# Kernel tuning notes

Hardware: AMD Instinct MI355X
Metric: run time of the kernel (lower is better)

The kernel has to match this reference:

```python
import jax, jax.numpy as jnp
import numpy as np

B, DIM, Hs, Ws_ = 16, 96, 112, 112
HEADS, WS, OUT = 3, 7, 96
DH = OUT // HEADS


def _rel_index(ws):
    ch = np.arange(ws)
    coords = np.stack(np.meshgrid(ch, ch, indexing='ij'), 0).reshape(2, -1)
    rel = (coords[:, :, None] - coords[:, None, :]).transpose(1, 2, 0).copy()
    rel[..., 0] += ws - 1
    rel[..., 1] += ws - 1
    rel[..., 0] *= 2 * ws - 1
    return rel.sum(-1)  # [ws*ws, ws*ws]


def grid_sample_zeros(img, grid):
    # img [N,C,H,W], grid [N,Hg,Wg,2] with (x,y) in [-1,1]; bilinear, align_corners=True, zeros padding
    N, C, H, W = img.shape
    x = (grid[..., 0] + 1.0) * 0.5 * (W - 1)
    y = (grid[..., 1] + 1.0) * 0.5 * (H - 1)
    x0 = jnp.floor(x); y0 = jnp.floor(y)
    x1 = x0 + 1.0; y1 = y0 + 1.0
    wa = (x1 - x) * (y1 - y); wb = (x - x0) * (y1 - y)
    wc = (x1 - x) * (y - y0); wd = (x - x0) * (y - y0)

    def gather(ix, iy):
        valid = ((ix >= 0) & (ix <= W - 1) & (iy >= 0) & (iy <= H - 1)).astype(img.dtype)
        ixc = jnp.clip(ix, 0, W - 1).astype(jnp.int32)
        iyc = jnp.clip(iy, 0, H - 1).astype(jnp.int32)
        vals = jax.vmap(lambda im, yy, xx: im[:, yy, xx])(img, iyc, ixc)  # [N,C,Hg,Wg]
        return vals * valid[:, None, :, :]

    return (gather(x0, y0) * wa[:, None] + gather(x1, y0) * wb[:, None]
            + gather(x0, y1) * wc[:, None] + gather(x1, y1) * wd[:, None])


def setup_inputs() -> dict:
    key = jax.random.key(0)
    ks = jax.random.split(key, 8)
    s = 0.02
    return {
        'x': jax.random.normal(ks[0], (B, DIM, Hs, Ws_), jnp.float32),
        'w_qkv': jax.random.normal(ks[1], (3 * OUT, DIM), jnp.float32) * s,
        'b_qkv': jnp.zeros((3 * OUT,), jnp.float32),
        'w_off': jax.random.normal(ks[2], (2 * HEADS, DIM), jnp.float32) * s,
        'b_off': jnp.zeros((2 * HEADS,), jnp.float32),
        'w_scl': jax.random.normal(ks[3], (2 * HEADS, DIM), jnp.float32) * s,
        'b_scl': jnp.zeros((2 * HEADS,), jnp.float32),
        'rpb': jax.random.normal(ks[4], ((2 * WS - 1) ** 2, HEADS), jnp.float32) * s,
        'w_proj': jax.random.normal(ks[5], (OUT, OUT), jnp.float32) * s,
        'b_proj': jnp.zeros((OUT,), jnp.float32),
    }


def _forward(x, w_qkv, b_qkv, w_off, b_off, w_scl, b_scl, rpb, w_proj, b_proj):
    b, C, h, w = x.shape
    ws, H, dh = WS, HEADS, DH
    scale = (C // H) ** -0.5
    pad_td = (ws - h % ws) % ws; pad_lr = (ws - w % ws) % ws
    pt, pd = pad_td // 2, pad_td - pad_td // 2
    pl, pr = pad_lr // 2, pad_lr - pad_lr // 2
    eh, ew = h + pad_td, w + pad_lr
    wnh, wnw = eh // ws, ew // ws
    xp = jnp.pad(x, ((0, 0), (0, 0), (pt, pd), (pl, pr)))

    # base reference grid, channel 0 = x (width), channel 1 = y (height)
    irh = jnp.linspace(-1.0, 1.0, eh); irw = jnp.linspace(-1.0, 1.0, ew)
    base = jnp.stack([jnp.broadcast_to(irw[None, :], (eh, ew)),
                      jnp.broadcast_to(irh[:, None], (eh, ew))], 0).reshape(2, wnh, ws, wnw, ws)
    bch = jnp.arange(ws) * 2.0 / (eh - 1); bch = bch - bch.mean()
    bcw = jnp.arange(ws) * 2.0 / (ew - 1); bcw = bcw - bcw.mean()
    wc = jnp.stack([jnp.broadcast_to(bcw[None, None, None, :], (wnh, ws, wnw, ws)),
                    jnp.broadcast_to(bch[None, :, None, None], (wnh, ws, wnw, ws))], 0)

    # per-window offset / scale prediction: avgpool(ws) -> leaky_relu -> 1x1 conv
    pooled = xp.reshape(b, C, wnh, ws, wnw, ws).mean(axis=(3, 5))
    act = jax.nn.leaky_relu(pooled)  # slope 0.01, matches torch default
    off = (jnp.einsum('bchw,oc->bohw', act, w_off) + b_off[None, :, None, None]).reshape(b * H, 2, wnh, wnw)
    off = jnp.stack([off[:, 0] / (h // ws), off[:, 1] / (w // ws)], 1)
    scl = (jnp.einsum('bchw,oc->bohw', act, w_scl) + b_scl[None, :, None, None]).reshape(b * H, 2, wnh, wnw)

    coords = base[None] + wc[None] * scl[:, :, :, None, :, None] + off[:, :, :, None, :, None]
    grid = coords.transpose(0, 2, 3, 4, 5, 1).reshape(b * H, eh, ew, 2)

    qkv = jnp.einsum('bchw,oc->bohw', x, w_qkv) + b_qkv[None, :, None, None]
    qkv = qkv.reshape(b, 3, H, dh, h, w).transpose(1, 0, 2, 3, 4, 5).reshape(3 * b * H, dh, h, w)
    qkv = jnp.pad(qkv, ((0, 0), (0, 0), (pt, pd), (pl, pr))).reshape(3, b * H, dh, eh, ew)
    q, k, v = qkv[0], qkv[1], qkv[2]

    k_s = grid_sample_zeros(k, grid)
    v_s = grid_sample_zeros(v, grid)

    def to_win(t):  # [b*H, dh, eh, ew] -> [b*wnh*wnw, H, ws*ws, dh]
        return t.reshape(b, H, dh, wnh, ws, wnw, ws).transpose(0, 3, 5, 1, 4, 6, 2).reshape(b * wnh * wnw, H, ws * ws, dh)

    qw, kw, vw = to_win(q), to_win(k_s), to_win(v_s)
    dots = jnp.einsum('wnqd,wnkd->wnqk', qw, kw) * scale
    rel_idx = jnp.asarray(_rel_index(ws))
    bias = rpb[rel_idx.reshape(-1)].reshape(ws * ws, ws * ws, H).transpose(2, 0, 1)
    attn = jax.nn.softmax(dots + bias[None], axis=-1)
    out = jnp.einsum('wnqk,wnkd->wnqd', attn, vw)
    out = out.reshape(b, wnh, wnw, H, ws, ws, dh).transpose(0, 3, 6, 1, 4, 2, 5).reshape(b, H * dh, eh, ew)
    out = out[:, :, pt:h + pt, pl:w + pl]
    out = jnp.einsum('bchw,oc->bohw', out, w_proj) + b_proj[None, :, None, None]
    return out


def reference(x, w_qkv, b_qkv, w_off, b_off, w_scl, b_scl, rpb, w_proj, b_proj):
    return _forward(x, w_qkv, b_qkv, w_off, b_off, w_scl, b_scl, rpb, w_proj, b_proj)
```

## Files before the change

kernel.cpp:

```cpp
#include <hip/hip_runtime.h>
#include <hip/hip_bf16.h>
#include <stdint.h>

#define NB 16
#define CDIM 96
#define HW 112
#define NPOS (HW*HW)
#define NHEAD 3
#define DH 32
#define WN 16
#define NWIN (WN*WN)
#define SCALE 0.17677669529663687f

typedef __attribute__((ext_vector_type(8))) short bf16x8;
typedef __attribute__((ext_vector_type(4))) float f32x4;

__device__ __forceinline__ float bfbits_lo(uint32_t w){ union{uint32_t u; float f;} a; a.u = w<<16; return a.f; }
__device__ __forceinline__ float bfbits_hi(uint32_t w){ union{uint32_t u; float f;} a; a.u = w & 0xFFFF0000u; return a.f; }
__device__ __forceinline__ uint32_t packbf(float x, float y){
  union{float f; uint32_t u;} a, b; a.f = x; b.f = y;
  uint32_t ua = a.u + 0x7FFFu + ((a.u>>16)&1u);
  uint32_t ub = b.u + 0x7FFFu + ((b.u>>16)&1u);
  return (ua>>16) | (ub & 0xFFFF0000u);
}
__device__ __forceinline__ unsigned short f2bf(float x){
  union{float f; uint32_t u;} a; a.f = x;
  return (unsigned short)((a.u + 0x7FFFu + ((a.u>>16)&1u))>>16);
}

__global__ void k_pool_act(const float* __restrict__ x, float* __restrict__ act){
  int n = blockIdx.x*256 + threadIdx.x;
  int ww = n & 15; int wh = (n>>4)&15; int bc = n>>8;
  const float* src = x + (size_t)bc*NPOS + (size_t)(wh*7)*HW + ww*7;
  float s = 0.f;
  #pragma unroll
  for (int r=0;r<7;r++){
    const float* row = src + r*HW;
    s += row[0]+row[1]+row[2]+row[3]+row[4]+row[5]+row[6];
  }
  s *= (1.f/49.f);
  act[n] = s > 0.f ? s : 0.01f*s;
}

__global__ void k_offscl(const float* __restrict__ act,
                         const float* __restrict__ woff, const float* __restrict__ boff,
                         const float* __restrict__ wscl, const float* __restrict__ bscl,
                         float4* __restrict__ offscl){
  int n = blockIdx.x*256 + threadIdx.x;
  int b = n >> 8; int wpos = n & 255;
  float accO[6], accS[6];
  #pragma unroll
  for (int o=0;o<6;o++){ accO[o]=boff[o]; accS[o]=bscl[o]; }
  const float* a = act + (size_t)b*CDIM*NWIN + wpos;
  for (int c=0;c<CDIM;c++){
    float av = a[(size_t)c*NWIN];
    #pragma unroll
    for (int o=0;o<6;o++){ accO[o] += av*woff[o*CDIM+c]; accS[o] += av*wscl[o*CDIM+c]; }
  }
  #pragma unroll
  for (int h=0;h<NHEAD;h++){
    float4 r;
    r.x = accO[2*h]   * (1.f/16.f);
    r.y = accO[2*h+1] * (1.f/16.f);
    r.z = accS[2*h];
    r.w = accS[2*h+1];
    offscl[(size_t)(b*NHEAD+h)*NWIN + wpos] = r;
  }
}

__global__ void k_bias_pre(const float* __restrict__ rpb, float* __restrict__ bias_g){
  int n = blockIdx.x*256 + threadIdx.x;
  if (n >= 3*64*64) return;
  int h = n >> 12; int q = (n>>6)&63; int k = n&63;
  float v = -1e30f;
  if (k < 49){
    int qc = q < 49 ? q : 48;
    int qi = qc/7, qj = qc - (qc/7)*7;
    int ki = k/7,  kj = k - (k/7)*7;
    v = rpb[((qi-ki+6)*13 + (qj-kj+6))*3 + h];
  }
  bias_g[n] = v;
}

__launch_bounds__(256)
__global__ void k_qkv_mfma(const float* __restrict__ x, const float* __restrict__ wqkv,
                           const float* __restrict__ bqkv,
                           unsigned short* __restrict__ q, unsigned short* __restrict__ kk,
                           unsigned short* __restrict__ v){
  __shared__ float xf[96*72];
  __shared__ uint4 xbf4[64*13];
  __shared__ uint4 wbf4[96*13];
  const int t = threadIdx.x;
  const int b = blockIdx.x / 196;
  const int p0 = (blockIdx.x % 196) * 64;

  #pragma unroll
  for (int i=0;i<6;i++){
    int f = t + i*256; int c = f>>4; int p4 = (f&15)*4;
    *(float4*)(xf + c*72 + p4) = *(const float4*)(x + (size_t)(b*CDIM+c)*NPOS + p0 + p4);
  }
  __syncthreads();
  #pragma unroll
  for (int i=0;i<3;i++){
    int u = t + i*256; int pos = u & 63; int oct = u >> 6;
    uint32_t pk0 = packbf(xf[(oct*8+0)*72+pos], xf[(oct*8+1)*72+pos]);
    uint32_t pk1 = packbf(xf[(oct*8+2)*72+pos], xf[(oct*8+3)*72+pos]);
    uint32_t pk2 = packbf(xf[(oct*8+4)*72+pos], xf[(oct*8+5)*72+pos]);
    uint32_t pk3 = packbf(xf[(oct*8+6)*72+pos], xf[(oct*8+7)*72+pos]);
    xbf4[pos*13 + oct] = make_uint4(pk0,pk1,pk2,pk3);
  }

  const int lane = t & 63, wv = t >> 6;
  const int g = lane >> 4, r16 = lane & 15;

  for (int s=0;s<3;s++){
    if (s) __syncthreads();
    #pragma unroll
    for (int i=0;i<9;i++){
      int f = t + i*256; int o = f/24; int c4m = f%24;
      float4 wvv = *(const float4*)(wqkv + (size_t)(s*96+o)*CDIM + c4m*4);
      ((uint2*)wbf4)[o*26 + c4m] = make_uint2(packbf(wvv.x,wvv.y), packbf(wvv.z,wvv.w));
    }
    __syncthreads();

    f32x4 acc[6];
    #pragma unroll
    for (int nf=0;nf<6;nf++) acc[nf] = (f32x4){0.f,0.f,0.f,0.f};
    #pragma unroll
    for (int ks=0;ks<3;ks++){
      bf16x8 a = *(const bf16x8*)&xbf4[(wv*16 + r16)*13 + ks*4 + g];
      #pragma unroll
      for (int nf=0;nf<6;nf++){
        bf16x8 bb = *(const bf16x8*)&wbf4[(nf*16 + r16)*13 + ks*4 + g];
        acc[nf] = __builtin_amdgcn_mfma_f32_16x16x32_bf16(a, bb, acc[nf], 0,0,0);
      }
    }
    unsigned short* dst = (s==0)?q:((s==1)?kk:v);
    float sc = (s==0) ? SCALE : 1.f;
    #pragma unroll
    for (int nf=0;nf<6;nf++){
      int o = nf*16 + r16; int h = o>>5; int d = o&31;
      float bv = bqkv[s*96+o];
      size_t base = ((size_t)(b*NHEAD+h)*NPOS + p0 + wv*16 + g*4)*DH + d;
      #pragma unroll
      for (int rr=0;rr<4;rr++)
        dst[base + (size_t)rr*DH] = f2bf((acc[nf][rr] + bv)*sc);
    }
  }
}

__launch_bounds__(128)
__global__ void k_attn_mfma(const unsigned short* __restrict__ qb,
                            const unsigned short* __restrict__ kb,
                            const unsigned short* __restrict__ vb,
                            const float4* __restrict__ offscl,
                            const float* __restrict__ bias_g,
                            float* __restrict__ aout){
  __shared__ unsigned short lds_u[2*8192];
  const int h   = blockIdx.x % 3;
  const int grp = blockIdx.x / 3;
  const int wv  = threadIdx.x >> 6;
  const int lane = threadIdx.x & 63;
  const int win = grp*2 + wv;
  const int b = win>>8, wh=(win>>4)&15, ww=win&15;
  const int bh = b*NHEAD + h;
  const int g = lane>>4, r16 = lane&15;

  unsigned short* K_s  = lds_u + wv*8192;
  unsigned short* VT_s = lds_u + wv*8192 + 2048;
  unsigned short* P_s  = lds_u + wv*8192 + 4096;

  uint4 qf[4];
  #pragma unroll
  for (int qt=0;qt<4;qt++){
    int qq = qt*16 + r16; if (qq > 48) qq = 48;
    int qi = qq/7; int qj = qq - qi*7;
    size_t pos = (size_t)(wh*7+qi)*HW + ww*7 + qj;
    qf[qt] = *(const uint4*)(qb + ((size_t)bh*NPOS + pos)*DH + g*8);
  }

  int ki = lane/7; int kj = lane - ki*7;
  uint32_t nbaddr[4]; float nbw[4];
  {
    float4 os = offscl[(size_t)bh*NWIN + (wh*16+ww)];
    float px = (float)(ww*7+kj) + (float)(kj-3)*os.z + 55.5f*os.x;
    float py = (float)(wh*7+ki) + (float)(ki-3)*os.w + 55.5f*os.y;
    float x0f = floorf(px), y0f = floorf(py);
    float fx = px-x0f, fy = py-y0f;
    int x0 = (int)x0f, y0 = (int)y0f;
    float wb[4] = {(1.f-fx)*(1.f-fy), fx*(1.f-fy), (1.f-fx)*fy, fx*fy};
    bool qok = lane < 49;
    #pragma unroll
    for (int nb=0;nb<4;nb++){
      int xi = x0 + (nb&1), yi = y0 + (nb>>1);
      int xc = min(max(xi,0),HW-1), yc = min(max(yi,0),HW-1);
      nbaddr[nb] = (uint32_t)(yc*HW + xc) * 64u;
      nbw[nb] = (qok && xi==xc && yi==yc) ? wb[nb] : 0.f;
    }
  }

  const char* kb8 = (const char*)kb + (size_t)bh*NPOS*64;
  const char* vb8 = (const char*)vb + (size_t)bh*NPOS*64;
  #pragma unroll
  for (int pp=0;pp<4;pp++){
    int spos = pp*16 + r16;
    float ka[8], va[8];
    #pragma unroll
    for (int j=0;j<8;j++){ ka[j]=0.f; va[j]=0.f; }
    #pragma unroll
    for (int nb=0;nb<4;nb++){
      uint32_t a = (uint32_t)__shfl((int)nbaddr[nb], spos);
      float    w = __shfl(nbw[nb], spos);
      uint4 uk = *(const uint4*)(kb8 + a + g*16);
      uint4 uv = *(const uint4*)(vb8 + a + g*16);
      ka[0]+=w*bfbits_lo(uk.x); ka[1]+=w*bfbits_hi(uk.x);
      ka[2]+=w*bfbits_lo(uk.y); ka[3]+=w*bfbits_hi(uk.y);
      ka[4]+=w*bfbits_lo(uk.z); ka[5]+=w*bfbits_hi(uk.z);
      ka[6]+=w*bfbits_lo(uk.w); ka[7]+=w*bfbits_hi(uk.w);
      va[0]+=w*bfbits_lo(uv.x); va[1]+=w*bfbits_hi(uv.x);
      va[2]+=w*bfbits_lo(uv.y); va[3]+=w*bfbits_hi(uv.y);
      va[4]+=w*bfbits_lo(uv.z); va[5]+=w*bfbits_hi(uv.z);
      va[6]+=w*bfbits_lo(uv.w); va[7]+=w*bfbits_hi(uv.w);
    }
    uint4 pk = make_uint4(packbf(ka[0],ka[1]), packbf(ka[2],ka[3]),
                          packbf(ka[4],ka[5]), packbf(ka[6],ka[7]));
    *(uint4*)&K_s[spos*32 + ((g ^ (spos&3))*8)] = pk;
    #pragma unroll
    for (int j=0;j<8;j++){
      int d = g*8 + j;
      VT_s[d*64 + (((spos>>3) ^ (d&7))*8) + (spos&7)] = f2bf(va[j]);
    }
  }

  __syncthreads();

  const float* bias_h = bias_g + h*4096;
  f32x4 acc[4][4];
  #pragma unroll
  for (int qt=0;qt<4;qt++){
    int qq = qt*16 + r16;
    #pragma unroll
    for (int at=0;at<4;at++)
      acc[at][qt] = *(const f32x4*)(bias_h + qq*64 + at*16 + g*4);
  }
  #pragma unroll
  for (int at=0;at<4;at++){
    bf16x8 a = *(const bf16x8*)&K_s[(at*16+r16)*32 + ((g ^ (r16&3))*8)];
    #pragma unroll
    for (int qt=0;qt<4;qt++)
      acc[at][qt] = __builtin_amdgcn_mfma_f32_16x16x32_bf16(a, *(const bf16x8*)&qf[qt], acc[at][qt], 0,0,0);
  }

  #pragma unroll
  for (int qt=0;qt<4;qt++){
    float m = acc[0][qt][0];
    #pragma unroll
    for (int at=0;at<4;at++)
      #pragma unroll
      for (int rr=0;rr<4;rr++) m = fmaxf(m, acc[at][qt][rr]);
    m = fmaxf(m, __shfl_xor(m, 16));
    m = fmaxf(m, __shfl_xor(m, 32));
    float s = 0.f;
    #pragma unroll
    for (int at=0;at<4;at++)
      #pragma unroll
      for (int rr=0;rr<4;rr++){ float e = __expf(acc[at][qt][rr]-m); acc[at][qt][rr]=e; s+=e; }
    s += __shfl_xor(s, 16);
    s += __shfl_xor(s, 32);
    float rl = 1.f/s;
    #pragma unroll
    for (int at=0;at<4;at++)
      #pragma unroll
      for (int rr=0;rr<4;rr++) acc[at][qt][rr] *= rl;
  }

  #pragma unroll
  for (int qt=0;qt<4;qt++){
    int qq = qt*16 + r16;
    #pragma unroll
    for (int at=0;at<4;at++){
      uint2 pk = make_uint2(packbf(acc[at][qt][0], acc[at][qt][1]),
                            packbf(acc[at][qt][2], acc[at][qt][3]));
      *(uint2*)&P_s[qq*64 + (((2*at + (g>>1)) ^ (qq&7))*8) + 4*(g&1)] = pk;
    }
  }

  __syncthreads();

  f32x4 o[4][2];
  #pragma unroll
  for (int mt=0;mt<4;mt++){ o[mt][0]=(f32x4){0,0,0,0}; o[mt][1]=(f32x4){0,0,0,0}; }
  #pragma unroll
  for (int kt=0;kt<2;kt++){
    bf16x8 bfr[2];
    #pragma unroll
    for (int nt=0;nt<2;nt++){
      int dh = nt*16 + r16;
      bfr[nt] = *(const bf16x8*)&VT_s[dh*64 + (((4*kt+g) ^ (r16&7))*8)];
    }
    #pragma unroll
    for (int mt=0;mt<4;mt++){
      int qq = mt*16 + r16;
      bf16x8 a = *(const bf16x8*)&P_s[qq*64 + (((4*kt+g) ^ (r16&7))*8)];
      o[mt][0] = __builtin_amdgcn_mfma_f32_16x16x32_bf16(a, bfr[0], o[mt][0], 0,0,0);
      o[mt][1] = __builtin_amdgcn_mfma_f32_16x16x32_bf16(a, bfr[1], o[mt][1], 0,0,0);
    }
  }

  float* outbase = aout + ((size_t)b*CDIM + h*DH)*NPOS;
  #pragma unroll
  for (int mt=0;mt<4;mt++){
    #pragma unroll
    for (int rr=0;rr<4;rr++){
      int qq = mt*16 + 4*g + rr;
      if (qq < 49){
        int qi = qq/7; int qj = qq - qi*7;
        size_t sp = (size_t)(wh*7+qi)*HW + ww*7 + qj;
        outbase[(size_t)r16*NPOS + sp]      = o[mt][0][rr];
        outbase[(size_t)(16+r16)*NPOS + sp] = o[mt][1][rr];
      }
    }
  }
}

__launch_bounds__(256)
__global__ void k_proj_mfma(const float* yin, const float* __restrict__ wproj,
                            const float* __restrict__ bproj, float* yout){
  __shared__ float xf[96*72];
  __shared__ uint4 xbf4[64*13];
  __shared__ uint4 wbf4[96*13];
  const int t = threadIdx.x;
  const int b = blockIdx.x / 196;
  const int p0 = (blockIdx.x % 196) * 64;

  #pragma unroll
  for (int i=0;i<6;i++){
    int f = t + i*256; int c = f>>4; int p4 = (f&15)*4;
    *(float4*)(xf + c*72 + p4) = *(const float4*)(yin + (size_t)(b*CDIM+c)*NPOS + p0 + p4);
  }
  __syncthreads();
  #pragma unroll
  for (int i=0;i<3;i++){
    int u = t + i*256; int pos = u & 63; int oct = u >> 6;
    uint32_t pk0 = packbf(xf[(oct*8+0)*72+pos], xf[(oct*8+1)*72+pos]);
    uint32_t pk1 = packbf(xf[(oct*8+2)*72+pos], xf[(oct*8+3)*72+pos]);
    uint32_t pk2 = packbf(xf[(oct*8+4)*72+pos], xf[(oct*8+5)*72+pos]);
    uint32_t pk3 = packbf(xf[(oct*8+6)*72+pos], xf[(oct*8+7)*72+pos]);
    xbf4[pos*13 + oct] = make_uint4(pk0,pk1,pk2,pk3);
  }
  #pragma unroll
  for (int i=0;i<9;i++){
    int f = t + i*256; int o = f/24; int c4m = f%24;
    float4 wvv = *(const float4*)(wproj + (size_t)o*CDIM + c4m*4);
    ((uint2*)wbf4)[o*26 + c4m] = make_uint2(packbf(wvv.x,wvv.y), packbf(wvv.z,wvv.w));
  }
  __syncthreads();

  const int lane = t & 63, wv = t >> 6;
  const int g = lane >> 4, r16 = lane & 15;
  f32x4 acc[6];
  #pragma unroll
  for (int nf=0;nf<6;nf++) acc[nf] = (f32x4){0.f,0.f,0.f,0.f};
  #pragma unroll
  for (int ks=0;ks<3;ks++){
    bf16x8 a = *(const bf16x8*)&xbf4[(wv*16 + r16)*13 + ks*4 + g];
    #pragma unroll
    for (int nf=0;nf<6;nf++){
      bf16x8 bb = *(const bf16x8*)&wbf4[(nf*16 + r16)*13 + ks*4 + g];
      acc[nf] = __builtin_amdgcn_mfma_f32_16x16x32_bf16(a, bb, acc[nf], 0,0,0);
    }
  }
  #pragma unroll
  for (int nf=0;nf<6;nf++){
    int o = nf*16 + r16;
    float bv = bproj[o];
    float* dst = yout + (size_t)(b*CDIM+o)*NPOS + p0 + wv*16 + g*4;
    #pragma unroll
    for (int rr=0;rr<4;rr++) dst[rr] = acc[nf][rr] + bv;
  }
}

extern "C" void kernel_launch(void* const* d_in, const int* in_sizes, int n_in,
                              void* d_out, int out_size, void* d_ws, size_t ws_size,
                              hipStream_t stream) {
  const float* x      = (const float*)d_in[0];
  const float* w_qkv  = (const float*)d_in[1];
  const float* b_qkv  = (const float*)d_in[2];
  const float* w_off  = (const float*)d_in[3];
  const float* b_off  = (const float*)d_in[4];
  const float* w_scl  = (const float*)d_in[5];
  const float* b_scl  = (const float*)d_in[6];
  const float* rpb    = (const float*)d_in[7];
  const float* w_proj = (const float*)d_in[8];
  const float* b_proj = (const float*)d_in[9];

  char* ws = (char*)d_ws;
  float*   act    = (float*)(ws + 0);
  float4*  offscl = (float4*)(ws + 1572864);
  float*   bias_g = (float*)(ws + 1769472);
  const size_t QKV_BYTES = (size_t)NB*NHEAD*NPOS*DH*2;
  unsigned short* qbuf = (unsigned short*)(ws + 2097152);
  unsigned short* kbuf = (unsigned short*)(ws + 2097152 + QKV_BYTES);
  unsigned short* vbuf = (unsigned short*)(ws + 2097152 + 2*QKV_BYTES);

  hipLaunchKernelGGL(k_pool_act,  dim3(1536), dim3(256), 0, stream, x, act);
  hipLaunchKernelGGL(k_offscl,    dim3(16),   dim3(256), 0, stream, act, w_off, b_off, w_scl, b_scl, offscl);
  hipLaunchKernelGGL(k_bias_pre,  dim3(48),   dim3(256), 0, stream, rpb, bias_g);
  hipLaunchKernelGGL(k_qkv_mfma,  dim3(16*196), dim3(256), 0, stream, x, w_qkv, b_qkv, qbuf, kbuf, vbuf);
  hipLaunchKernelGGL(k_attn_mfma, dim3(3*2048), dim3(128), 0, stream,
                     qbuf, kbuf, vbuf, offscl, bias_g, (float*)d_out);
  hipLaunchKernelGGL(k_proj_mfma, dim3(16*196), dim3(256), 0, stream,
                     (const float*)d_out, w_proj, b_proj, (float*)d_out);
}
```

Baseline: 242.4 us.

## Keep K and P fragments in registers, reshuffle P via lane shuffles

The attention kernel now keeps the sampled K tile in registers as the MFMA operand instead of writing it to LDS and reading it back. The softmax probabilities are repacked into the PV MFMA operand layout with cross-lane shuffles, and the PV product is computed transposed (V^T as A operand). This removes the P LDS buffer and a block barrier and cuts LDS from 32KB to 8KB per block, which may raise occupancy. The cost is more shuffle instructions and register pressure, and the output store pattern changes to per-lane channel-strided writes.

```diff
diff --git a/kernel.cpp b/kernel.cpp
--- a/kernel.cpp
+++ b/kernel.cpp
@@ -156,7 +156,7 @@
                             const float4* __restrict__ offscl,
                             const float* __restrict__ bias_g,
                             float* __restrict__ aout){
-  __shared__ unsigned short lds_u[2*8192];
+  __shared__ unsigned short VT_all[2*2048];
   const int h   = blockIdx.x % 3;
   const int grp = blockIdx.x / 3;
   const int wv  = threadIdx.x >> 6;
@@ -165,10 +165,7 @@
   const int b = win>>8, wh=(win>>4)&15, ww=win&15;
   const int bh = b*NHEAD + h;
   const int g = lane>>4, r16 = lane&15;
-
-  unsigned short* K_s  = lds_u + wv*8192;
-  unsigned short* VT_s = lds_u + wv*8192 + 2048;
-  unsigned short* P_s  = lds_u + wv*8192 + 4096;
+  unsigned short* VT_s = VT_all + wv*2048;
 
   uint4 qf[4];
   #pragma unroll
@@ -201,6 +198,7 @@
 
   const char* kb8 = (const char*)kb + (size_t)bh*NPOS*64;
   const char* vb8 = (const char*)vb + (size_t)bh*NPOS*64;
+  uint4 kfrag[4];
   #pragma unroll
   for (int pp=0;pp<4;pp++){
     int spos = pp*16 + r16;
@@ -222,9 +220,8 @@
       va[4]+=w*bfbits_lo(uv.z); va[5]+=w*bfbits_hi(uv.z);
       va[6]+=w*bfbits_lo(uv.w); va[7]+=w*bfbits_hi(uv.w);
     }
-    uint4 pk = make_uint4(packbf(ka[0],ka[1]), packbf(ka[2],ka[3]),
-                          packbf(ka[4],ka[5]), packbf(ka[6],ka[7]));
-    *(uint4*)&K_s[spos*32 + ((g ^ (spos&3))*8)] = pk;
+    kfrag[pp] = make_uint4(packbf(ka[0],ka[1]), packbf(ka[2],ka[3]),
+                           packbf(ka[4],ka[5]), packbf(ka[6],ka[7]));
     #pragma unroll
     for (int j=0;j<8;j++){
       int d = g*8 + j;
@@ -232,7 +229,9 @@
     }
   }
 
+  __builtin_amdgcn_sched_barrier(0);
   __syncthreads();
+  __builtin_amdgcn_sched_barrier(0);
 
   const float* bias_h = bias_g + h*4096;
   f32x4 acc[4][4];
@@ -245,7 +244,7 @@
   }
   #pragma unroll
   for (int at=0;at<4;at++){
-    bf16x8 a = *(const bf16x8*)&K_s[(at*16+r16)*32 + ((g ^ (r16&3))*8)];
+    bf16x8 a = *(const bf16x8*)&kfrag[at];
     #pragma unroll
     for (int qt=0;qt<4;qt++)
       acc[at][qt] = __builtin_amdgcn_mfma_f32_16x16x32_bf16(a, *(const bf16x8*)&qf[qt], acc[at][qt], 0,0,0);
@@ -274,51 +273,64 @@
       for (int rr=0;rr<4;rr++) acc[at][qt][rr] *= rl;
   }
 
+  uint32_t plo[4][4], phi[4][4];
+  #pragma unroll
+  for (int at=0;at<4;at++)
+    #pragma unroll
+    for (int qt=0;qt<4;qt++){
+      plo[at][qt] = packbf(acc[at][qt][0], acc[at][qt][1]);
+      phi[at][qt] = packbf(acc[at][qt][2], acc[at][qt][3]);
+    }
+
+  f32x4 o[2][4];
+  #pragma unroll
+  for (int dt=0;dt<2;dt++)
+    #pragma unroll
+    for (int qt=0;qt<4;qt++) o[dt][qt] = (f32x4){0.f,0.f,0.f,0.f};
+
+  #pragma unroll
+  for (int kt=0;kt<2;kt++){
+    uint4 pfrag[4];
+    const int s0 = ((2*g)&3)*16 + r16;
+    const int s1 = ((2*g+1)&3)*16 + r16;
+    const bool odd = (g & 2);
+    #pragma unroll
+    for (int qt=0;qt<4;qt++){
+      uint32_t e_lo0 = (uint32_t)__shfl((int)plo[2*kt  ][qt], s0);
+      uint32_t e_hi0 = (uint32_t)__shfl((int)phi[2*kt  ][qt], s0);
+      uint32_t e_lo1 = (uint32_t)__shfl((int)plo[2*kt  ][qt], s1);
+      uint32_t e_hi1 = (uint32_t)__shfl((int)phi[2*kt  ][qt], s1);
+      uint32_t o_lo0 = (uint32_t)__shfl((int)plo[2*kt+1][qt], s0);
+      uint32_t o_hi0 = (uint32_t)__shfl((int)phi[2*kt+1][qt], s0);
+      uint32_t o_lo1 = (uint32_t)__shfl((int)plo[2*kt+1][qt], s1);
+      uint32_t o_hi1 = (uint32_t)__shfl((int)phi[2*kt+1][qt], s1);
+      pfrag[qt] = make_uint4(odd?o_lo0:e_lo0, odd?o_hi0:e_hi0,
+                             odd?o_lo1:e_lo1, odd?o_hi1:e_hi1);
+    }
+    #pragma unroll
+    for (int dt=0;dt<2;dt++){
+      int d = dt*16 + r16;
+      bf16x8 a = *(const bf16x8*)&VT_s[d*64 + (((kt*4+g) ^ (d&7))*8)];
+      #pragma unroll
+      for (int qt=0;qt<4;qt++)
+        o[dt][qt] = __builtin_amdgcn_mfma_f32_16x16x32_bf16(a, *(const bf16x8*)&pfrag[qt], o[dt][qt], 0,0,0);
+    }
+  }
+
+  float* outb = aout + ((size_t)b*CDIM + h*DH)*NPOS;
   #pragma unroll
   for (int qt=0;qt<4;qt++){
-    int qq = qt*16 + r16;
-    #pragma unroll
-    for (int at=0;at<4;at++){
-      uint2 pk = make_uint2(packbf(acc[at][qt][0], acc[at][qt][1]),
-                            packbf(acc[at][qt][2], acc[at][qt][3]));
-      *(uint2*)&P_s[qq*64 + (((2*at + (g>>1)) ^ (qq&7))*8) + 4*(g&1)] = pk;
-    }
-  }
-
-  __syncthreads();
-
-  f32x4 o[4][2];
-  #pragma unroll
-  for (int mt=0;mt<4;mt++){ o[mt][0]=(f32x4){0,0,0,0}; o[mt][1]=(f32x4){0,0,0,0}; }
-  #pragma unroll
-  for (int kt=0;kt<2;kt++){
-    bf16x8 bfr[2];
-    #pragma unroll
-    for (int nt=0;nt<2;nt++){
-      int dh = nt*16 + r16;
-      bfr[nt] = *(const bf16x8*)&VT_s[dh*64 + (((4*kt+g) ^ (r16&7))*8)];
-    }
-    #pragma unroll
-    for (int mt=0;mt<4;mt++){
-      int qq = mt*16 + r16;
-      bf16x8 a = *(const bf16x8*)&P_s[qq*64 + (((4*kt+g) ^ (r16&7))*8)];
-      o[mt][0] = __builtin_amdgcn_mfma_f32_16x16x32_bf16(a, bfr[0], o[mt][0], 0,0,0);
-      o[mt][1] = __builtin_amdgcn_mfma_f32_16x16x32_bf16(a, bfr[1], o[mt][1], 0,0,0);
-    }
-  }
-
-  float* outbase = aout + ((size_t)b*CDIM + h*DH)*NPOS;
-  #pragma unroll
-  for (int mt=0;mt<4;mt++){
-    #pragma unroll
-    for (int rr=0;rr<4;rr++){
-      int qq = mt*16 + 4*g + rr;
-      if (qq < 49){
-        int qi = qq/7; int qj = qq - qi*7;
-        size_t sp = (size_t)(wh*7+qi)*HW + ww*7 + qj;
-        outbase[(size_t)r16*NPOS + sp]      = o[mt][0][rr];
-        outbase[(size_t)(16+r16)*NPOS + sp] = o[mt][1][rr];
-      }
+    int q = qt*16 + r16;
+    if (q < 49){
+      int qi = q/7; int qj = q - qi*7;
+      size_t opix = (size_t)(wh*7+qi)*HW + ww*7 + qj;
+      #pragma unroll
+      for (int dt=0;dt<2;dt++)
+        #pragma unroll
+        for (int rr=0;rr<4;rr++){
+          int d = dt*16 + g*4 + rr;
+          outb[(size_t)d*NPOS + opix] = o[dt][qt][rr];
+        }
     }
   }
 }
```

Result: faster. 209.6 us (-13.6%).
